# Performance work log

Hardware: AMD Instinct MI355X
Metric: run time of the kernel (lower is better)

## Reference

```python
import jax, jax.numpy as jnp
import numpy as np

N = 1048576  # rays * samples per batch
IN_DIM = 32          # hashgrid encoder output (16 levels x 2 feats)
SH_DIM = 16          # degree-4 spherical harmonics
HID = 64
GEO = 15


def sh_encode(v):
    """Real spherical harmonics up to degree 4 (16 comps), v: [N,3] unit vecs."""
    x, y, z = v[..., 0], v[..., 1], v[..., 2]
    xx, yy, zz = x * x, y * y, z * z
    xy, yz, xz = x * y, y * z, x * z
    comps = [
        jnp.full_like(x, 0.28209479177387814),
        -0.48860251190291987 * y,
        0.48860251190291987 * z,
        -0.48860251190291987 * x,
        1.0925484305920792 * xy,
        -1.0925484305920792 * yz,
        0.94617469575755997 * zz - 0.31539156525252005,
        -1.0925484305920792 * xz,
        0.54627421529603959 * (xx - yy),
        0.59004358992664352 * y * (3.0 * xx - yy),
        2.8906114426405538 * xy * z,
        0.45704579946446572 * y * (4.0 * zz - xx - yy),
        0.3731763325901154 * z * (2.0 * zz - 3.0 * xx - 3.0 * yy),
        0.45704579946446572 * x * (4.0 * zz - xx - yy),
        1.445305721320277 * z * (xx - yy),
        0.5900435899266435 * x * (xx - 3.0 * yy),
    ]
    return jnp.stack(comps, axis=-1)


def _w(key, fan_in, fan_out):
    return jax.random.normal(key, (fan_in, fan_out), dtype=jnp.float32) / np.sqrt(fan_in)


def setup_inputs() -> dict:
    key = jax.random.key(0)
    ks = jax.random.split(key, 12)
    x_feat = jax.random.normal(ks[0], (N, IN_DIM), dtype=jnp.float32)
    d = jax.random.normal(ks[1], (N, 3), dtype=jnp.float32)
    d = d / jnp.linalg.norm(d, axis=-1, keepdims=True)
    lig = jax.random.normal(ks[2], (N, 3), dtype=jnp.float32)
    lig = lig / jnp.linalg.norm(lig, axis=-1, keepdims=True)
    return {
        "x_feat": x_feat, "d": d, "lig": lig,
        # sigma net: 32 -> 64 -> 1+15
        "w_sig0": _w(ks[3], IN_DIM, HID),
        "w_sig1": _w(ks[4], HID, 1 + GEO),
        # color net: (16+16+32) -> 64, (64+15) -> 64, 64 -> 3
        "w_col0": _w(ks[5], SH_DIM + SH_DIM + IN_DIM, HID),
        "w_col1": _w(ks[6], HID + GEO, HID),
        "w_col2": _w(ks[7], HID, 3),
        # vis net (only 2 layers run in forward): (16+32) -> 64, 64 -> 1
        "w_vis0": _w(ks[8], SH_DIM + IN_DIM, HID),
        "w_vis1": _w(ks[9], HID, 1),
    }


def reference(x_feat, d, lig, w_sig0, w_sig1, w_col0, w_col1, w_col2, w_vis0, w_vis1):
    # sigma tower (bias-free)
    h = jax.nn.relu(x_feat @ w_sig0)
    h = h @ w_sig1                      # [N, 1+GEO]
    geo_feat = h[..., 1:]               # sigma = trunc_exp(h[...,0]) is unused in output

    d_enc = sh_encode(d)                # [N,16]
    l_enc = sh_encode(lig)              # [N,16]

    # color tower: cat([h_x, light, d]) then cat geo_feat before layer 1
    hc = jnp.concatenate([x_feat, l_enc, d_enc], axis=-1)
    hc = jax.nn.relu(hc @ w_col0)
    hc = jnp.concatenate([hc, geo_feat], axis=-1)
    hc = jax.nn.relu(hc @ w_col1)
    hc = hc @ w_col2
    color = jax.nn.relu(hc)             # [N,3]

    # vis tower: cat([h_x, light]), 2 layers (range(num_layers))
    hv = jnp.concatenate([x_feat, l_enc], axis=-1)
    hv = jax.nn.relu(hv @ w_vis0)
    hv = hv @ w_vis1
    vis = jax.nn.sigmoid(hv)            # [N,1]

    return color * vis                  # broadcast -> [N,3]
```

## Files before the change

### kernel.cpp

```cpp
#include <hip/hip_runtime.h>
#include <math.h>

#define BLOCK 256
#define GRID  512

typedef _Float16 half8 __attribute__((ext_vector_type(8)));
typedef float    f32x4 __attribute__((ext_vector_type(4)));

__device__ __forceinline__ int phi(int nt, int m) {
    return ((nt >> 1) << 5) + ((m >> 2) << 3) + ((nt & 1) << 2) + (m & 3);
}

__device__ __forceinline__ half8 bfragW(const float* __restrict__ w, int N0,
                                        int nsrc, int k0, int Kreal, bool valid) {
    half8 r;
    #pragma unroll
    for (int j = 0; j < 8; j++) {
        int k = k0 + j;
        float v = (valid && k < Kreal) ? w[k * N0 + nsrc] : 0.f;
        r[j] = (_Float16)v;
    }
    return r;
}

__device__ __forceinline__ half8 packrelu(f32x4 a, f32x4 b) {
    half8 h;
    #pragma unroll
    for (int r = 0; r < 4; r++) {
        h[r]     = (_Float16)fmaxf(a[r], 0.f);
        h[4 + r] = (_Float16)fmaxf(b[r], 0.f);
    }
    return h;
}

__device__ __forceinline__ half8 packraw(f32x4 a, f32x4 b) {
    half8 h;
    #pragma unroll
    for (int r = 0; r < 4; r++) {
        h[r]     = (_Float16)a[r];
        h[4 + r] = (_Float16)b[r];
    }
    return h;
}

__device__ __forceinline__ void sh16(float x, float y, float z, float* e) {
    float xx = x * x, yy = y * y, zz = z * z;
    float xy = x * y, yz = y * z, xz = x * z;
    e[0]  = 0.28209479177387814f;
    e[1]  = -0.48860251190291987f * y;
    e[2]  = 0.48860251190291987f * z;
    e[3]  = -0.48860251190291987f * x;
    e[4]  = 1.0925484305920792f * xy;
    e[5]  = -1.0925484305920792f * yz;
    e[6]  = 0.94617469575756f * zz - 0.31539156525252005f;
    e[7]  = -1.0925484305920792f * xz;
    e[8]  = 0.5462742152960396f * (xx - yy);
    e[9]  = 0.5900435899266435f * y * (3.0f * xx - yy);
    e[10] = 2.890611442640554f * xy * z;
    e[11] = 0.4570457994644657f * y * (4.0f * zz - xx - yy);
    e[12] = 0.3731763325901154f * z * (2.0f * zz - 3.0f * xx - 3.0f * yy);
    e[13] = 0.4570457994644657f * x * (4.0f * zz - xx - yy);
    e[14] = 1.445305721320277f * z * (xx - yy);
    e[15] = 0.5900435899266435f * x * (xx - 3.0f * yy);
}

#define MFMA(A, B, C) __builtin_amdgcn_mfma_f32_16x16x32_f16((A), (B), (C), 0, 0, 0)

__global__ __launch_bounds__(BLOCK, 2) void nerf_reg(
    const float* __restrict__ x_feat,
    const float* __restrict__ dvec,
    const float* __restrict__ lvec,
    const float* __restrict__ w_sig0,
    const float* __restrict__ w_sig1,
    const float* __restrict__ w_col0,
    const float* __restrict__ w_col1,
    const float* __restrict__ w_col2,
    const float* __restrict__ w_vis0,
    const float* __restrict__ w_vis1,
    float* __restrict__ out, int n)
{
    const int tid  = threadIdx.x;
    const int wv   = tid >> 6;
    const int lane = tid & 63;
    const int m    = lane & 15;
    const int q    = lane >> 4;

    half8 Wsig0[4], Wcol0[8], Wvis0[8], Wsig1[4], Wvis1[2], Wcol1[12], Wcol2[2];
    #pragma unroll
    for (int nt = 0; nt < 4; nt++)
        Wsig0[nt] = bfragW(w_sig0, 64, phi(nt, m), q * 8, 32, true);
    #pragma unroll
    for (int nt = 0; nt < 4; nt++)
        #pragma unroll
        for (int kt = 0; kt < 2; kt++)
            Wcol0[nt * 2 + kt] = bfragW(w_col0, 64, phi(nt, m), kt * 32 + q * 8, 64, true);
    #pragma unroll
    for (int nt = 0; nt < 4; nt++)
        #pragma unroll
        for (int kt = 0; kt < 2; kt++)
            Wvis0[nt * 2 + kt] = bfragW(w_vis0, 64, phi(nt, m), kt * 32 + q * 8, 48, true);
    #pragma unroll
    for (int nt = 0; nt < 2; nt++)
        #pragma unroll
        for (int kt = 0; kt < 2; kt++) {
            int g = ((m >> 2) << 3) + ((nt & 1) << 2) + (m & 3);
            bool valid = ((m >> 2) < 2) && (g < 15);
            Wsig1[nt * 2 + kt] = bfragW(w_sig1, 16, g + 1, kt * 32 + q * 8, 64, valid);
        }
    #pragma unroll
    for (int kt = 0; kt < 2; kt++)
        Wvis1[kt] = bfragW(w_vis1, 1, 0, kt * 32 + q * 8, 64, m == 0);
    #pragma unroll
    for (int nt = 0; nt < 4; nt++)
        #pragma unroll
        for (int kt = 0; kt < 3; kt++)
            Wcol1[nt * 3 + kt] = bfragW(w_col1, 64, phi(nt, m), kt * 32 + q * 8, 79, true);
    #pragma unroll
    for (int kt = 0; kt < 2; kt++)
        Wcol2[kt] = bfragW(w_col2, 3, m, kt * 32 + q * 8, 64, m < 3);

    const f32x4 z = {0.f, 0.f, 0.f, 0.f};
    const int ntiles = n >> 6;
    for (int t = blockIdx.x; t < ntiles; t += GRID) {
        const int pt = (t << 6) + wv * 16 + m;

        const float4* xv = (const float4*)(x_feat + (size_t)pt * 32 + q * 8);
        float4 v0 = xv[0], v1 = xv[1];
        half8 fI0;
        fI0[0] = (_Float16)v0.x; fI0[1] = (_Float16)v0.y;
        fI0[2] = (_Float16)v0.z; fI0[3] = (_Float16)v0.w;
        fI0[4] = (_Float16)v1.x; fI0[5] = (_Float16)v1.y;
        fI0[6] = (_Float16)v1.z; fI0[7] = (_Float16)v1.w;

        const float* vv = (q < 2 ? lvec : dvec) + (size_t)pt * 3;
        float e[16];
        sh16(vv[0], vv[1], vv[2], e);
        half8 lo, hi;
        #pragma unroll
        for (int u = 0; u < 8; u++) {
            lo[u] = (_Float16)e[u];
            hi[u] = (_Float16)e[8 + u];
        }
        half8 fI1 = (q & 1) ? hi : lo;

        f32x4 a0 = z, a1 = z, a2 = z, a3 = z;
        a0 = MFMA(Wsig0[0], fI0, a0);
        a1 = MFMA(Wsig0[1], fI0, a1);
        a2 = MFMA(Wsig0[2], fI0, a2);
        a3 = MFMA(Wsig0[3], fI0, a3);
        half8 hK0 = packrelu(a0, a1), hK1 = packrelu(a2, a3);

        a0 = z; a1 = z; a2 = z; a3 = z;
        a0 = MFMA(Wcol0[0], fI0, a0); a0 = MFMA(Wcol0[1], fI1, a0);
        a1 = MFMA(Wcol0[2], fI0, a1); a1 = MFMA(Wcol0[3], fI1, a1);
        a2 = MFMA(Wcol0[4], fI0, a2); a2 = MFMA(Wcol0[5], fI1, a2);
        a3 = MFMA(Wcol0[6], fI0, a3); a3 = MFMA(Wcol0[7], fI1, a3);
        half8 cK0 = packrelu(a0, a1), cK1 = packrelu(a2, a3);

        a0 = z; a1 = z; a2 = z; a3 = z;
        a0 = MFMA(Wvis0[0], fI0, a0); a0 = MFMA(Wvis0[1], fI1, a0);
        a1 = MFMA(Wvis0[2], fI0, a1); a1 = MFMA(Wvis0[3], fI1, a1);
        a2 = MFMA(Wvis0[4], fI0, a2); a2 = MFMA(Wvis0[5], fI1, a2);
        a3 = MFMA(Wvis0[6], fI0, a3); a3 = MFMA(Wvis0[7], fI1, a3);
        half8 vK0 = packrelu(a0, a1), vK1 = packrelu(a2, a3);

        a0 = z; a1 = z;
        a0 = MFMA(Wsig1[0], hK0, a0); a0 = MFMA(Wsig1[1], hK1, a0);
        a1 = MFMA(Wsig1[2], hK0, a1); a1 = MFMA(Wsig1[3], hK1, a1);
        half8 gK2 = packraw(a0, a1);

        f32x4 av = z;
        av = MFMA(Wvis1[0], vK0, av);
        av = MFMA(Wvis1[1], vK1, av);
        float vis = 1.f / (1.f + expf(-av[0]));

        a0 = z; a1 = z; a2 = z; a3 = z;
        a0 = MFMA(Wcol1[0], cK0, a0); a0 = MFMA(Wcol1[1], cK1, a0); a0 = MFMA(Wcol1[2], gK2, a0);
        a1 = MFMA(Wcol1[3], cK0, a1); a1 = MFMA(Wcol1[4], cK1, a1); a1 = MFMA(Wcol1[5], gK2, a1);
        a2 = MFMA(Wcol1[6], cK0, a2); a2 = MFMA(Wcol1[7], cK1, a2); a2 = MFMA(Wcol1[8], gK2, a2);
        a3 = MFMA(Wcol1[9], cK0, a3); a3 = MFMA(Wcol1[10], cK1, a3); a3 = MFMA(Wcol1[11], gK2, a3);
        half8 h2K0 = packrelu(a0, a1), h2K1 = packrelu(a2, a3);

        f32x4 ac = z;
        ac = MFMA(Wcol2[0], h2K0, ac);
        ac = MFMA(Wcol2[1], h2K1, ac);
        if (q == 0) {
            float* o = out + (size_t)pt * 3;
            o[0] = fmaxf(ac[0], 0.f) * vis;
            o[1] = fmaxf(ac[1], 0.f) * vis;
            o[2] = fmaxf(ac[2], 0.f) * vis;
        }
    }
}

extern "C" void kernel_launch(void* const* d_in, const int* in_sizes, int n_in,
                              void* d_out, int out_size, void* d_ws, size_t ws_size,
                              hipStream_t stream) {
    const float* x_feat = (const float*)d_in[0];
    const float* dvec   = (const float*)d_in[1];
    const float* lvec   = (const float*)d_in[2];
    const float* w_sig0 = (const float*)d_in[3];
    const float* w_sig1 = (const float*)d_in[4];
    const float* w_col0 = (const float*)d_in[5];
    const float* w_col1 = (const float*)d_in[6];
    const float* w_col2 = (const float*)d_in[7];
    const float* w_vis0 = (const float*)d_in[8];
    const float* w_vis1 = (const float*)d_in[9];
    float* out = (float*)d_out;

    const int n = in_sizes[0] / 32;
    nerf_reg<<<GRID, BLOCK, 0, stream>>>(x_feat, dvec, lvec,
                                         w_sig0, w_sig1, w_col0, w_col1,
                                         w_col2, w_vis0, w_vis1, out, n);
}
```

Baseline: 292.0 us.

## Stage MLP weight fragments in LDS and prefetch next tile inputs

Moves the 40 per-lane fp16 weight fragments out of registers into shared memory, built cooperatively once per block. This frees VGPRs, so launch bounds rise to 4 blocks per SM and the grid doubles. It also software-prefetches the next tile's features and direction vectors before the MFMA chain, overlapping global loads with compute. In exchange every MFMA now needs an LDS read of its weight operand, adding LDS traffic and latency to the inner loop.

Result: slower. 459.2 us (+57.3%).

```diff
diff --git a/kernel.cpp b/kernel.cpp
--- a/kernel.cpp
+++ b/kernel.cpp
@@ -2,7 +2,7 @@
 #include <math.h>
 
 #define BLOCK 256
-#define GRID  512
+#define GRID  1024
 
 typedef _Float16 half8 __attribute__((ext_vector_type(8)));
 typedef float    f32x4 __attribute__((ext_vector_type(4)));
@@ -64,9 +64,47 @@
     e[15] = 0.5900435899266435f * x * (xx - 3.0f * yy);
 }
 
+#define F_SIG0 0
+#define F_COL0 4
+#define F_VIS0 12
+#define F_SIG1 20
+#define F_VIS1 24
+#define F_COL1 26
+#define F_COL2 38
+
+__device__ half8 build_frag(int f, int m, int q,
+                            const float* w_sig0, const float* w_sig1,
+                            const float* w_col0, const float* w_col1,
+                            const float* w_col2, const float* w_vis0,
+                            const float* w_vis1) {
+    if (f < 4) {
+        return bfragW(w_sig0, 64, phi(f, m), q * 8, 32, true);
+    } else if (f < 12) {
+        int i = f - 4, nt = i >> 1, kt = i & 1;
+        return bfragW(w_col0, 64, phi(nt, m), kt * 32 + q * 8, 64, true);
+    } else if (f < 20) {
+        int i = f - 12, nt = i >> 1, kt = i & 1;
+        return bfragW(w_vis0, 64, phi(nt, m), kt * 32 + q * 8, 48, true);
+    } else if (f < 24) {
+        int i = f - 20, nt = i >> 1, kt = i & 1;
+        int g = ((m >> 2) << 3) + ((nt & 1) << 2) + (m & 3);
+        bool valid = ((m >> 2) < 2) && (g < 15);
+        return bfragW(w_sig1, 16, g + 1, kt * 32 + q * 8, 64, valid);
+    } else if (f < 26) {
+        int kt = f - 24;
+        return bfragW(w_vis1, 1, 0, kt * 32 + q * 8, 64, m == 0);
+    } else if (f < 38) {
+        int i = f - 26, nt = i / 3, kt = i % 3;
+        return bfragW(w_col1, 64, phi(nt, m), kt * 32 + q * 8, 79, true);
+    } else {
+        int kt = f - 38;
+        return bfragW(w_col2, 3, m, kt * 32 + q * 8, 64, m < 3);
+    }
+}
+
 #define MFMA(A, B, C) __builtin_amdgcn_mfma_f32_16x16x32_f16((A), (B), (C), 0, 0, 0)
 
-__global__ __launch_bounds__(BLOCK, 2) void nerf_reg(
+__global__ __launch_bounds__(BLOCK, 4) void nerf_lds(
     const float* __restrict__ x_feat,
     const float* __restrict__ dvec,
     const float* __restrict__ lvec,
@@ -79,62 +117,47 @@
     const float* __restrict__ w_vis1,
     float* __restrict__ out, int n)
 {
+    __shared__ half8 sWf[40 * 64];
+
     const int tid  = threadIdx.x;
     const int wv   = tid >> 6;
     const int lane = tid & 63;
     const int m    = lane & 15;
     const int q    = lane >> 4;
 
-    half8 Wsig0[4], Wcol0[8], Wvis0[8], Wsig1[4], Wvis1[2], Wcol1[12], Wcol2[2];
-    #pragma unroll
-    for (int nt = 0; nt < 4; nt++)
-        Wsig0[nt] = bfragW(w_sig0, 64, phi(nt, m), q * 8, 32, true);
-    #pragma unroll
-    for (int nt = 0; nt < 4; nt++)
-        #pragma unroll
-        for (int kt = 0; kt < 2; kt++)
-            Wcol0[nt * 2 + kt] = bfragW(w_col0, 64, phi(nt, m), kt * 32 + q * 8, 64, true);
-    #pragma unroll
-    for (int nt = 0; nt < 4; nt++)
-        #pragma unroll
-        for (int kt = 0; kt < 2; kt++)
-            Wvis0[nt * 2 + kt] = bfragW(w_vis0, 64, phi(nt, m), kt * 32 + q * 8, 48, true);
-    #pragma unroll
-    for (int nt = 0; nt < 2; nt++)
-        #pragma unroll
-        for (int kt = 0; kt < 2; kt++) {
-            int g = ((m >> 2) << 3) + ((nt & 1) << 2) + (m & 3);
-            bool valid = ((m >> 2) < 2) && (g < 15);
-            Wsig1[nt * 2 + kt] = bfragW(w_sig1, 16, g + 1, kt * 32 + q * 8, 64, valid);
-        }
-    #pragma unroll
-    for (int kt = 0; kt < 2; kt++)
-        Wvis1[kt] = bfragW(w_vis1, 1, 0, kt * 32 + q * 8, 64, m == 0);
-    #pragma unroll
-    for (int nt = 0; nt < 4; nt++)
-        #pragma unroll
-        for (int kt = 0; kt < 3; kt++)
-            Wcol1[nt * 3 + kt] = bfragW(w_col1, 64, phi(nt, m), kt * 32 + q * 8, 79, true);
-    #pragma unroll
-    for (int kt = 0; kt < 2; kt++)
-        Wcol2[kt] = bfragW(w_col2, 3, m, kt * 32 + q * 8, 64, m < 3);
-
+    for (int f = wv; f < 40; f += 4)
+        sWf[f * 64 + lane] = build_frag(f, m, q, w_sig0, w_sig1, w_col0,
+                                        w_col1, w_col2, w_vis0, w_vis1);
+    __syncthreads();
+
+    const half8* W = sWf;
     const f32x4 z = {0.f, 0.f, 0.f, 0.f};
     const int ntiles = n >> 6;
-    for (int t = blockIdx.x; t < ntiles; t += GRID) {
+
+    int t = blockIdx.x;
+    if (t >= ntiles) return;
+
+    float4 pv0, pv1;
+    float pe0, pe1, pe2;
+    {
         const int pt = (t << 6) + wv * 16 + m;
-
         const float4* xv = (const float4*)(x_feat + (size_t)pt * 32 + q * 8);
-        float4 v0 = xv[0], v1 = xv[1];
+        pv0 = xv[0]; pv1 = xv[1];
+        const float* vvp = (q < 2 ? lvec : dvec) + (size_t)pt * 3;
+        pe0 = vvp[0]; pe1 = vvp[1]; pe2 = vvp[2];
+    }
+
+    while (t < ntiles) {
+        const int pt = (t << 6) + wv * 16 + m;
+
         half8 fI0;
-        fI0[0] = (_Float16)v0.x; fI0[1] = (_Float16)v0.y;
-        fI0[2] = (_Float16)v0.z; fI0[3] = (_Float16)v0.w;
-        fI0[4] = (_Float16)v1.x; fI0[5] = (_Float16)v1.y;
-        fI0[6] = (_Float16)v1.z; fI0[7] = (_Float16)v1.w;
-
-        const float* vv = (q < 2 ? lvec : dvec) + (size_t)pt * 3;
+        fI0[0] = (_Float16)pv0.x; fI0[1] = (_Float16)pv0.y;
+        fI0[2] = (_Float16)pv0.z; fI0[3] = (_Float16)pv0.w;
+        fI0[4] = (_Float16)pv1.x; fI0[5] = (_Float16)pv1.y;
+        fI0[6] = (_Float16)pv1.z; fI0[7] = (_Float16)pv1.w;
+
         float e[16];
-        sh16(vv[0], vv[1], vv[2], e);
+        sh16(pe0, pe1, pe2, e);
         half8 lo, hi;
         #pragma unroll
         for (int u = 0; u < 8; u++) {
@@ -143,53 +166,83 @@
         }
         half8 fI1 = (q & 1) ? hi : lo;
 
+        const int tn = t + GRID;
+        {
+            const int tp = (tn < ntiles) ? tn : t;
+            const int ptn = (tp << 6) + wv * 16 + m;
+            const float4* xv = (const float4*)(x_feat + (size_t)ptn * 32 + q * 8);
+            pv0 = xv[0]; pv1 = xv[1];
+            const float* vvp = (q < 2 ? lvec : dvec) + (size_t)ptn * 3;
+            pe0 = vvp[0]; pe1 = vvp[1]; pe2 = vvp[2];
+        }
+
         f32x4 a0 = z, a1 = z, a2 = z, a3 = z;
-        a0 = MFMA(Wsig0[0], fI0, a0);
-        a1 = MFMA(Wsig0[1], fI0, a1);
-        a2 = MFMA(Wsig0[2], fI0, a2);
-        a3 = MFMA(Wsig0[3], fI0, a3);
+        a0 = MFMA(W[(F_SIG0 + 0) * 64 + lane], fI0, a0);
+        a1 = MFMA(W[(F_SIG0 + 1) * 64 + lane], fI0, a1);
+        a2 = MFMA(W[(F_SIG0 + 2) * 64 + lane], fI0, a2);
+        a3 = MFMA(W[(F_SIG0 + 3) * 64 + lane], fI0, a3);
         half8 hK0 = packrelu(a0, a1), hK1 = packrelu(a2, a3);
 
         a0 = z; a1 = z; a2 = z; a3 = z;
-        a0 = MFMA(Wcol0[0], fI0, a0); a0 = MFMA(Wcol0[1], fI1, a0);
-        a1 = MFMA(Wcol0[2], fI0, a1); a1 = MFMA(Wcol0[3], fI1, a1);
-        a2 = MFMA(Wcol0[4], fI0, a2); a2 = MFMA(Wcol0[5], fI1, a2);
-        a3 = MFMA(Wcol0[6], fI0, a3); a3 = MFMA(Wcol0[7], fI1, a3);
+        a0 = MFMA(W[(F_COL0 + 0) * 64 + lane], fI0, a0);
+        a0 = MFMA(W[(F_COL0 + 1) * 64 + lane], fI1, a0);
+        a1 = MFMA(W[(F_COL0 + 2) * 64 + lane], fI0, a1);
+        a1 = MFMA(W[(F_COL0 + 3) * 64 + lane], fI1, a1);
+        a2 = MFMA(W[(F_COL0 + 4) * 64 + lane], fI0, a2);
+        a2 = MFMA(W[(F_COL0 + 5) * 64 + lane], fI1, a2);
+        a3 = MFMA(W[(F_COL0 + 6) * 64 + lane], fI0, a3);
+        a3 = MFMA(W[(F_COL0 + 7) * 64 + lane], fI1, a3);
         half8 cK0 = packrelu(a0, a1), cK1 = packrelu(a2, a3);
 
         a0 = z; a1 = z; a2 = z; a3 = z;
-        a0 = MFMA(Wvis0[0], fI0, a0); a0 = MFMA(Wvis0[1], fI1, a0);
-        a1 = MFMA(Wvis0[2], fI0, a1); a1 = MFMA(Wvis0[3], fI1, a1);
-        a2 = MFMA(Wvis0[4], fI0, a2); a2 = MFMA(Wvis0[5], fI1, a2);
-        a3 = MFMA(Wvis0[6], fI0, a3); a3 = MFMA(Wvis0[7], fI1, a3);
+        a0 = MFMA(W[(F_VIS0 + 0) * 64 + lane], fI0, a0);
+        a0 = MFMA(W[(F_VIS0 + 1) * 64 + lane], fI1, a0);
+        a1 = MFMA(W[(F_VIS0 + 2) * 64 + lane], fI0, a1);
+        a1 = MFMA(W[(F_VIS0 + 3) * 64 + lane], fI1, a1);
+        a2 = MFMA(W[(F_VIS0 + 4) * 64 + lane], fI0, a2);
+        a2 = MFMA(W[(F_VIS0 + 5) * 64 + lane], fI1, a2);
+        a3 = MFMA(W[(F_VIS0 + 6) * 64 + lane], fI0, a3);
+        a3 = MFMA(W[(F_VIS0 + 7) * 64 + lane], fI1, a3);
         half8 vK0 = packrelu(a0, a1), vK1 = packrelu(a2, a3);
 
         a0 = z; a1 = z;
-        a0 = MFMA(Wsig1[0], hK0, a0); a0 = MFMA(Wsig1[1], hK1, a0);
-        a1 = MFMA(Wsig1[2], hK0, a1); a1 = MFMA(Wsig1[3], hK1, a1);
+        a0 = MFMA(W[(F_SIG1 + 0) * 64 + lane], hK0, a0);
+        a0 = MFMA(W[(F_SIG1 + 1) * 64 + lane], hK1, a0);
+        a1 = MFMA(W[(F_SIG1 + 2) * 64 + lane], hK0, a1);
+        a1 = MFMA(W[(F_SIG1 + 3) * 64 + lane], hK1, a1);
         half8 gK2 = packraw(a0, a1);
 
         f32x4 av = z;
-        av = MFMA(Wvis1[0], vK0, av);
-        av = MFMA(Wvis1[1], vK1, av);
+        av = MFMA(W[(F_VIS1 + 0) * 64 + lane], vK0, av);
+        av = MFMA(W[(F_VIS1 + 1) * 64 + lane], vK1, av);
         float vis = 1.f / (1.f + expf(-av[0]));
 
         a0 = z; a1 = z; a2 = z; a3 = z;
-        a0 = MFMA(Wcol1[0], cK0, a0); a0 = MFMA(Wcol1[1], cK1, a0); a0 = MFMA(Wcol1[2], gK2, a0);
-        a1 = MFMA(Wcol1[3], cK0, a1); a1 = MFMA(Wcol1[4], cK1, a1); a1 = MFMA(Wcol1[5], gK2, a1);
-        a2 = MFMA(Wcol1[6], cK0, a2); a2 = MFMA(Wcol1[7], cK1, a2); a2 = MFMA(Wcol1[8], gK2, a2);
-        a3 = MFMA(Wcol1[9], cK0, a3); a3 = MFMA(Wcol1[10], cK1, a3); a3 = MFMA(Wcol1[11], gK2, a3);
+        a0 = MFMA(W[(F_COL1 + 0) * 64 + lane], cK0, a0);
+        a0 = MFMA(W[(F_COL1 + 1) * 64 + lane], cK1, a0);
+        a0 = MFMA(W[(F_COL1 + 2) * 64 + lane], gK2, a0);
+        a1 = MFMA(W[(F_COL1 + 3) * 64 + lane], cK0, a1);
+        a1 = MFMA(W[(F_COL1 + 4) * 64 + lane], cK1, a1);
+        a1 = MFMA(W[(F_COL1 + 5) * 64 + lane], gK2, a1);
+        a2 = MFMA(W[(F_COL1 + 6) * 64 + lane], cK0, a2);
+        a2 = MFMA(W[(F_COL1 + 7) * 64 + lane], cK1, a2);
+        a2 = MFMA(W[(F_COL1 + 8) * 64 + lane], gK2, a2);
+        a3 = MFMA(W[(F_COL1 + 9) * 64 + lane], cK0, a3);
+        a3 = MFMA(W[(F_COL1 + 10) * 64 + lane], cK1, a3);
+        a3 = MFMA(W[(F_COL1 + 11) * 64 + lane], gK2, a3);
         half8 h2K0 = packrelu(a0, a1), h2K1 = packrelu(a2, a3);
 
         f32x4 ac = z;
-        ac = MFMA(Wcol2[0], h2K0, ac);
-        ac = MFMA(Wcol2[1], h2K1, ac);
+        ac = MFMA(W[(F_COL2 + 0) * 64 + lane], h2K0, ac);
+        ac = MFMA(W[(F_COL2 + 1) * 64 + lane], h2K1, ac);
         if (q == 0) {
             float* o = out + (size_t)pt * 3;
             o[0] = fmaxf(ac[0], 0.f) * vis;
             o[1] = fmaxf(ac[1], 0.f) * vis;
             o[2] = fmaxf(ac[2], 0.f) * vis;
         }
+
+        t = tn;
     }
 }
 
@@ -209,7 +262,7 @@
     float* out = (float*)d_out;
 
     const int n = in_sizes[0] / 32;
-    nerf_reg<<<GRID, BLOCK, 0, stream>>>(x_feat, dvec, lvec,
+    nerf_lds<<<GRID, BLOCK, 0, stream>>>(x_feat, dvec, lvec,
                                          w_sig0, w_sig1, w_col0, w_col1,
                                          w_col2, w_vis0, w_vis1, out, n);
 }
```
